# Performance work log

Measured on AMD Instinct MI355X. Metric: run time of the kernel, lower is better.

Reference implementation:

```python
import jax, jax.numpy as jnp
import numpy as np

NUM_SELECT = 300

def _cxcywh_to_xyxy(b):
    cx, cy, w, h = b[..., 0], b[..., 1], b[..., 2], b[..., 3]
    return jnp.stack([cx - w * 0.5, cy - h * 0.5, cx + w * 0.5, cy + h * 0.5], axis=-1)

def setup_inputs() -> dict:
    key = jax.random.key(0)
    k1, k2, k3 = jax.random.split(key, 3)
    B, Q, C = 512, 900, 256
    pred_logits = jax.random.normal(k1, (B, Q, C), dtype=jnp.float32)
    pred_boxes = jax.random.uniform(k2, (B, Q, 4), dtype=jnp.float32)  # normalized cxcywh in [0,1)
    target_sizes = jax.random.uniform(k3, (B, 2), dtype=jnp.float32) * 1333.0 + 1.0  # (h, w)
    return {"pred_logits": pred_logits, "pred_boxes": pred_boxes, "target_sizes": target_sizes}

def reference(pred_logits, pred_boxes, target_sizes):
    B, Q, C = pred_logits.shape
    prob = jax.nn.sigmoid(pred_logits)                      # [B,Q,C]
    flat = prob.reshape(B, Q * C)
    topk_vals, topk_idxs = jax.lax.top_k(flat, NUM_SELECT)  # [B,K]
    scores = topk_vals
    topk_boxes = topk_idxs // C                              # query index
    labels = topk_idxs % C                                   # class index
    out_boxes = _cxcywh_to_xyxy(pred_boxes)                  # [B,Q,4]
    out_boxes = jnp.take_along_axis(out_boxes, topk_boxes[:, :, None], axis=1)  # [B,K,4]
    img_h, img_w = target_sizes[:, 0], target_sizes[:, 1]
    scale = jnp.stack([img_w, img_h, img_w, img_h], axis=1)  # [B,4]
    out_boxes = out_boxes * scale[:, None, :]
    return scores, labels, out_boxes
```

## Files before the change

### kernel.cpp

```cpp
#include <hip/hip_runtime.h>
#include <math.h>


#define NB 512
#define NQ 900
#define NC 256
#define NELEM (NQ*NC)
#define NF4 (NELEM/4)
#define NSEL 300
#define NTHREADS 1024
#define CAP1 6144
#define CAP2 1024
#define SORT_N 1024

__device__ __forceinline__ unsigned keyOf(float f) {
    unsigned u = __float_as_uint(f);
    return u ^ ((unsigned)((int)u >> 31) | 0x80000000u);
}
__device__ __forceinline__ float keyToFloat(unsigned k) {
    unsigned u = (k & 0x80000000u) ? (k ^ 0x80000000u) : ~k;
    return __uint_as_float(u);
}

__global__ __launch_bounds__(NTHREADS) void detpost_kernel(
    const float* __restrict__ logits, const float* __restrict__ boxes,
    const float* __restrict__ tsizes, float* __restrict__ out)
{
    __shared__ uint2 buf1[CAP1];
    __shared__ uint2 buf2[CAP2];
    __shared__ unsigned hist[256];
    __shared__ unsigned sAbove, sCnt, sT, sCand, sDone;

    const int tid  = threadIdx.x;
    const int lane = tid & 63;
    const int row  = blockIdx.x;
    const float4* row4 = (const float4*)(logits + (size_t)row * NELEM);

    unsigned P = 0, pos = 28, T = 0, cand = 0;
    while (true) {
        if (tid < 16) hist[tid] = 0;
        if (tid == 16 % NTHREADS + 16) {}
        if (tid == 17) sAbove = 0;
        __syncthreads();

        unsigned c[16];
        #pragma unroll
        for (int n = 0; n < 16; ++n) c[n] = 0;
        unsigned cAb = 0;
        const unsigned long long upper = (unsigned long long)P + (16ULL << pos);
        unsigned long long acc = 0; int pend = 0;

        for (unsigned i = tid; i < NF4; i += NTHREADS) {
            float4 v = row4[i];
            #pragma unroll
            for (int c4 = 0; c4 < 4; ++c4) {
                float f = (c4 == 0) ? v.x : (c4 == 1) ? v.y : (c4 == 2) ? v.z : v.w;
                unsigned k = keyOf(f);
                if ((unsigned long long)k >= upper) cAb++;
                else if (k >= P) acc += 1ULL << (((k >> pos) & 0xFu) << 2);
            }
            if (++pend == 3) {
                pend = 0;
                #pragma unroll
                for (int n = 0; n < 16; ++n) c[n] += (unsigned)(acc >> (4 * n)) & 0xFu;
                acc = 0;
            }
        }
        #pragma unroll
        for (int n = 0; n < 16; ++n) c[n] += (unsigned)(acc >> (4 * n)) & 0xFu;

        #pragma unroll
        for (int n = 0; n < 16; ++n) {
            unsigned v = c[n];
            for (int off = 32; off; off >>= 1) v += __shfl_down(v, off, 64);
            if (lane == 0 && v) atomicAdd(&hist[n], v);
        }
        {
            unsigned v = cAb;
            for (int off = 32; off; off >>= 1) v += __shfl_down(v, off, 64);
            if (lane == 0 && v) atomicAdd(&sAbove, v);
        }
        __syncthreads();

        if (tid == 0) {
            unsigned run = sAbove; int b = 0;
            for (int n = 15; n >= 0; --n) {
                run += hist[n];
                if (run >= NSEL) { b = n; break; }
            }
            sT = P | ((unsigned)b << pos);
            sCand = run;
            sDone = (run <= CAP1 || pos == 0) ? 1u : 0u;
        }
        __syncthreads();
        T = sT; cand = sCand;
        unsigned done = sDone;
        __syncthreads();
        if (done) break;
        P = T; pos -= 4;
    }

    if (tid == 0) sCnt = 0;
    __syncthreads();
    for (unsigned i = tid; i < NF4; i += NTHREADS) {
        float4 v = row4[i];
        #pragma unroll
        for (int c4 = 0; c4 < 4; ++c4) {
            float f = (c4 == 0) ? v.x : (c4 == 1) ? v.y : (c4 == 2) ? v.z : v.w;
            unsigned k = keyOf(f);
            if (k >= T) {
                unsigned p2 = atomicAdd(&sCnt, 1u);
                if (p2 < CAP1) buf1[p2] = make_uint2(k, i * 4u + (unsigned)c4);
            }
        }
    }
    __syncthreads();
    unsigned cnt = min(sCnt, (unsigned)CAP1);
    (void)cand;

    uint2* src = buf1; uint2* dst = buf2;
    unsigned dstCap = CAP2;
    int p = (int)pos - 8;
    while (cnt > CAP2 && p >= 0) {
        if (tid < 256) hist[tid] = 0;
        if (tid == 0) { sAbove = 0; sCnt = 0; }
        __syncthreads();

        const unsigned Pm = T & (0xFFFFFFFFu << (p + 8));
        const unsigned long long up = (unsigned long long)Pm + (1ULL << (p + 8));
        for (unsigned i = tid; i < cnt; i += NTHREADS) {
            unsigned k = src[i].x;
            if ((unsigned long long)k >= up) atomicAdd(&sAbove, 1u);
            else atomicAdd(&hist[(k >> p) & 0xFFu], 1u);
        }
        __syncthreads();

        if (tid == 0) {
            unsigned run = sAbove; int b = 0;
            for (int n = 255; n >= 0; --n) {
                run += hist[n];
                if (run >= NSEL) { b = n; break; }
            }
            sT = Pm | ((unsigned)b << p);
            sCand = run;
        }
        __syncthreads();
        const unsigned Tn = sT;
        const unsigned newCnt = min(sCand, dstCap);
        for (unsigned i = tid; i < cnt; i += NTHREADS) {
            uint2 e = src[i];
            if (e.x >= Tn) {
                unsigned q = atomicAdd(&sCnt, 1u);
                if (q < dstCap) dst[q] = e;
            }
        }
        __syncthreads();
        T = Tn; cnt = newCnt;
        uint2* t = src; src = dst; dst = t;
        dstCap = (dst == buf1) ? (unsigned)CAP1 : (unsigned)CAP2;
        p -= 8;
    }
    if (cnt > CAP2) cnt = CAP2;

    unsigned long long* zb = (unsigned long long*)buf1;
    {
        unsigned i = tid;
        unsigned long long z = 0;
        if (i < cnt) {
            uint2 e = src[i];
            z = ((unsigned long long)e.x << 32) | (unsigned)(~e.y);
        }
        zb[i] = z;
    }
    __syncthreads();
    for (unsigned kk = 2; kk <= SORT_N; kk <<= 1) {
        for (unsigned j = kk >> 1; j > 0; j >>= 1) {
            unsigned i = tid, ixj = i ^ j;
            if (ixj > i) {
                unsigned long long a = zb[i], bz = zb[ixj];
                bool sw = ((i & kk) == 0) ? (a < bz) : (a > bz);
                if (sw) { zb[i] = bz; zb[ixj] = a; }
            }
            __syncthreads();
        }
    }

    if (tid < NSEL) {
        unsigned long long z = zb[tid];
        unsigned k   = (unsigned)(z >> 32);
        unsigned idx = ~(unsigned)z;
        float f = keyToFloat(k);
        double pd = 1.0 / (1.0 + exp(-(double)f));
        unsigned label = idx & (NC - 1);
        unsigned q = idx >> 8;
        float4 bx = ((const float4*)boxes)[(size_t)row * NQ + q];
        float imh = tsizes[row * 2 + 0];
        float imw = tsizes[row * 2 + 1];
        float x0 = (bx.x - bx.z * 0.5f) * imw;
        float y0 = (bx.y - bx.w * 0.5f) * imh;
        float x1 = (bx.x + bx.z * 0.5f) * imw;
        float y1 = (bx.y + bx.w * 0.5f) * imh;
        out[(size_t)row * NSEL + tid] = (float)pd;
        out[(size_t)NB * NSEL + (size_t)row * NSEL + tid] = (float)label;
        float* ob = out + (size_t)2 * NB * NSEL + ((size_t)row * NSEL + tid) * 4;
        ob[0] = x0; ob[1] = y0; ob[2] = x1; ob[3] = y1;
    }
}

extern "C" void kernel_launch(void* const* d_in, const int* in_sizes, int n_in,
                              void* d_out, int out_size, void* d_ws, size_t ws_size,
                              hipStream_t stream) {
    const float* logits = (const float*)d_in[0];
    const float* boxes  = (const float*)d_in[1];
    const float* tsz    = (const float*)d_in[2];
    float* out = (float*)d_out;
    detpost_kernel<<<NB, NTHREADS, 0, stream>>>(logits, boxes, tsz, out);
}
```

Measured before the change: 715.1 us.

## Replace 4-bit radix select passes with wide 8192-bin LDS histogram select

The multi-pass 4-bit radix select, which reads the full row once per pass, is replaced with a 13-bit (8192-bin) shared-memory histogram built with LDS atomics, followed by a parallel suffix scan to find the threshold bin. For typical logit distributions this should settle the threshold in one pass, so the row is read twice (histogram plus collect) instead of many times. The collect step writes packed 64-bit keys straight into a 2048-entry buffer, removing the shared-memory refinement loop, and the bitonic sort adapts between 1024 and 2048 entries. Loads are manually unrolled four float4s per iteration. The cost is heavy LDS atomic contention on popular bins and a larger sort when there are more than 1024 candidates.

```diff
diff --git a/kernel.cpp b/kernel.cpp
--- a/kernel.cpp
+++ b/kernel.cpp
@@ -8,10 +8,11 @@
 #define NELEM (NQ*NC)
 #define NF4 (NELEM/4)
 #define NSEL 300
-#define NTHREADS 1024
-#define CAP1 6144
-#define CAP2 1024
-#define SORT_N 1024
+#define NT 1024
+#define HBINS 8192
+#define CAP 2048
+
+typedef unsigned long long ull;
 
 __device__ __forceinline__ unsigned keyOf(float f) {
     unsigned u = __float_as_uint(f);
@@ -22,171 +23,132 @@
     return __uint_as_float(u);
 }
 
-__global__ __launch_bounds__(NTHREADS) void detpost_kernel(
+__global__ __launch_bounds__(NT) void detpost_kernel(
     const float* __restrict__ logits, const float* __restrict__ boxes,
     const float* __restrict__ tsizes, float* __restrict__ out)
 {
-    __shared__ uint2 buf1[CAP1];
-    __shared__ uint2 buf2[CAP2];
-    __shared__ unsigned hist[256];
-    __shared__ unsigned sAbove, sCnt, sT, sCand, sDone;
+    __shared__ unsigned hist[HBINS];
+    __shared__ ull zb[CAP];
+    __shared__ unsigned suf[NT];
+    __shared__ unsigned sT, sCand, sAbove, sDone, sCnt;
 
-    const int tid  = threadIdx.x;
-    const int lane = tid & 63;
-    const int row  = blockIdx.x;
-    const float4* row4 = (const float4*)(logits + (size_t)row * NELEM);
+    const int tid = threadIdx.x;
+    const int row = blockIdx.x;
+    const float4* __restrict__ r4 = (const float4*)(logits + (size_t)row * NELEM);
 
-    unsigned P = 0, pos = 28, T = 0, cand = 0;
+    unsigned W0 = 0;
+    unsigned sh = 19;
+    unsigned above = 0;
+    unsigned T, cand;
+
     while (true) {
-        if (tid < 16) hist[tid] = 0;
-        if (tid == 16 % NTHREADS + 16) {}
-        if (tid == 17) sAbove = 0;
+        for (int i = tid; i < HBINS; i += NT) hist[i] = 0;
         __syncthreads();
 
-        unsigned c[16];
-        #pragma unroll
-        for (int n = 0; n < 16; ++n) c[n] = 0;
-        unsigned cAb = 0;
-        const unsigned long long upper = (unsigned long long)P + (16ULL << pos);
-        unsigned long long acc = 0; int pend = 0;
-
-        for (unsigned i = tid; i < NF4; i += NTHREADS) {
-            float4 v = row4[i];
-            #pragma unroll
-            for (int c4 = 0; c4 < 4; ++c4) {
-                float f = (c4 == 0) ? v.x : (c4 == 1) ? v.y : (c4 == 2) ? v.z : v.w;
-                unsigned k = keyOf(f);
-                if ((unsigned long long)k >= upper) cAb++;
-                else if (k >= P) acc += 1ULL << (((k >> pos) & 0xFu) << 2);
-            }
-            if (++pend == 3) {
-                pend = 0;
-                #pragma unroll
-                for (int n = 0; n < 16; ++n) c[n] += (unsigned)(acc >> (4 * n)) & 0xFu;
-                acc = 0;
-            }
+        unsigned i0 = tid;
+        #pragma unroll 1
+        for (int it = 0; it < 14; ++it, i0 += 4096) {
+            float4 a = r4[i0];
+            float4 b = r4[i0 + 1024];
+            float4 c = r4[i0 + 2048];
+            float4 d = r4[i0 + 3072];
+            #define PH(f) { unsigned k = keyOf(f); unsigned bin = (k - W0) >> sh; \
+                            if (bin < HBINS) atomicAdd(&hist[bin], 1u); }
+            PH(a.x) PH(a.y) PH(a.z) PH(a.w)
+            PH(b.x) PH(b.y) PH(b.z) PH(b.w)
+            PH(c.x) PH(c.y) PH(c.z) PH(c.w)
+            PH(d.x) PH(d.y) PH(d.z) PH(d.w)
         }
-        #pragma unroll
-        for (int n = 0; n < 16; ++n) c[n] += (unsigned)(acc >> (4 * n)) & 0xFu;
-
-        #pragma unroll
-        for (int n = 0; n < 16; ++n) {
-            unsigned v = c[n];
-            for (int off = 32; off; off >>= 1) v += __shfl_down(v, off, 64);
-            if (lane == 0 && v) atomicAdd(&hist[n], v);
-        }
-        {
-            unsigned v = cAb;
-            for (int off = 32; off; off >>= 1) v += __shfl_down(v, off, 64);
-            if (lane == 0 && v) atomicAdd(&sAbove, v);
+        if (tid < 256) {
+            float4 a = r4[57344 + tid];
+            PH(a.x) PH(a.y) PH(a.z) PH(a.w)
         }
         __syncthreads();
 
-        if (tid == 0) {
-            unsigned run = sAbove; int b = 0;
-            for (int n = 15; n >= 0; --n) {
-                run += hist[n];
-                if (run >= NSEL) { b = n; break; }
+        unsigned local = 0;
+        #pragma unroll
+        for (int j = 0; j < 8; ++j) local += hist[tid * 8 + j];
+        suf[tid] = local;
+        __syncthreads();
+        for (int off = 1; off < NT; off <<= 1) {
+            unsigned v = suf[tid] + ((tid + off < NT) ? suf[tid + off] : 0u);
+            __syncthreads();
+            suf[tid] = v;
+            __syncthreads();
+        }
+        unsigned mySuf = suf[tid];
+        unsigned nxt = (tid < NT - 1) ? suf[tid + 1] : 0u;
+        if (above + mySuf >= NSEL && above + nxt < NSEL) {
+            unsigned run = above + nxt;
+            for (int j = 7; j >= 0; --j) {
+                unsigned h = hist[tid * 8 + j];
+                run += h;
+                if (run >= NSEL) {
+                    sT = W0 + ((unsigned)(tid * 8 + j) << sh);
+                    sCand = run;
+                    sAbove = run - h;
+                    sDone = (run <= CAP || sh == 0) ? 1u : 0u;
+                    break;
+                }
             }
-            sT = P | ((unsigned)b << pos);
-            sCand = run;
-            sDone = (run <= CAP1 || pos == 0) ? 1u : 0u;
         }
         __syncthreads();
         T = sT; cand = sCand;
-        unsigned done = sDone;
+        if (sDone) break;
+        above = sAbove;
+        W0 = T;
+        sh = (sh >= 13) ? (sh - 13) : 0u;
         __syncthreads();
-        if (done) break;
-        P = T; pos -= 4;
     }
+    (void)cand;
 
     if (tid == 0) sCnt = 0;
     __syncthreads();
-    for (unsigned i = tid; i < NF4; i += NTHREADS) {
-        float4 v = row4[i];
-        #pragma unroll
-        for (int c4 = 0; c4 < 4; ++c4) {
-            float f = (c4 == 0) ? v.x : (c4 == 1) ? v.y : (c4 == 2) ? v.z : v.w;
-            unsigned k = keyOf(f);
-            if (k >= T) {
-                unsigned p2 = atomicAdd(&sCnt, 1u);
-                if (p2 < CAP1) buf1[p2] = make_uint2(k, i * 4u + (unsigned)c4);
-            }
+    {
+        unsigned i0 = tid;
+        #pragma unroll 1
+        for (int it = 0; it < 14; ++it, i0 += 4096) {
+            float4 a = r4[i0];
+            float4 b = r4[i0 + 1024];
+            float4 c = r4[i0 + 2048];
+            float4 d = r4[i0 + 3072];
+            #define PC(f, ei) { unsigned k = keyOf(f); if (k >= T) { \
+                unsigned p = atomicAdd(&sCnt, 1u); \
+                if (p < CAP) zb[p] = ((ull)k << 32) | (unsigned)~(unsigned)(ei); } }
+            PC(a.x, i0*4+0)          PC(a.y, i0*4+1)          PC(a.z, i0*4+2)          PC(a.w, i0*4+3)
+            PC(b.x, (i0+1024)*4+0)   PC(b.y, (i0+1024)*4+1)   PC(b.z, (i0+1024)*4+2)   PC(b.w, (i0+1024)*4+3)
+            PC(c.x, (i0+2048)*4+0)   PC(c.y, (i0+2048)*4+1)   PC(c.z, (i0+2048)*4+2)   PC(c.w, (i0+2048)*4+3)
+            PC(d.x, (i0+3072)*4+0)   PC(d.y, (i0+3072)*4+1)   PC(d.z, (i0+3072)*4+2)   PC(d.w, (i0+3072)*4+3)
+        }
+        if (tid < 256) {
+            float4 a = r4[57344 + tid];
+            unsigned e0 = (57344 + tid) * 4;
+            PC(a.x, e0+0) PC(a.y, e0+1) PC(a.z, e0+2) PC(a.w, e0+3)
         }
     }
     __syncthreads();
-    unsigned cnt = min(sCnt, (unsigned)CAP1);
-    (void)cand;
+    unsigned cnt = min(sCnt, (unsigned)CAP);
 
-    uint2* src = buf1; uint2* dst = buf2;
-    unsigned dstCap = CAP2;
-    int p = (int)pos - 8;
-    while (cnt > CAP2 && p >= 0) {
-        if (tid < 256) hist[tid] = 0;
-        if (tid == 0) { sAbove = 0; sCnt = 0; }
-        __syncthreads();
-
-        const unsigned Pm = T & (0xFFFFFFFFu << (p + 8));
-        const unsigned long long up = (unsigned long long)Pm + (1ULL << (p + 8));
-        for (unsigned i = tid; i < cnt; i += NTHREADS) {
-            unsigned k = src[i].x;
-            if ((unsigned long long)k >= up) atomicAdd(&sAbove, 1u);
-            else atomicAdd(&hist[(k >> p) & 0xFFu], 1u);
-        }
-        __syncthreads();
-
-        if (tid == 0) {
-            unsigned run = sAbove; int b = 0;
-            for (int n = 255; n >= 0; --n) {
-                run += hist[n];
-                if (run >= NSEL) { b = n; break; }
-            }
-            sT = Pm | ((unsigned)b << p);
-            sCand = run;
-        }
-        __syncthreads();
-        const unsigned Tn = sT;
-        const unsigned newCnt = min(sCand, dstCap);
-        for (unsigned i = tid; i < cnt; i += NTHREADS) {
-            uint2 e = src[i];
-            if (e.x >= Tn) {
-                unsigned q = atomicAdd(&sCnt, 1u);
-                if (q < dstCap) dst[q] = e;
-            }
-        }
-        __syncthreads();
-        T = Tn; cnt = newCnt;
-        uint2* t = src; src = dst; dst = t;
-        dstCap = (dst == buf1) ? (unsigned)CAP1 : (unsigned)CAP2;
-        p -= 8;
-    }
-    if (cnt > CAP2) cnt = CAP2;
-
-    unsigned long long* zb = (unsigned long long*)buf1;
-    {
-        unsigned i = tid;
-        unsigned long long z = 0;
-        if (i < cnt) {
-            uint2 e = src[i];
-            z = ((unsigned long long)e.x << 32) | (unsigned)(~e.y);
-        }
-        zb[i] = z;
-    }
+    unsigned nSort = (cnt <= 1024u) ? 1024u : (unsigned)CAP;
+    for (unsigned i = tid; i < nSort; i += NT)
+        if (i >= cnt) zb[i] = 0ULL;
     __syncthreads();
-    for (unsigned kk = 2; kk <= SORT_N; kk <<= 1) {
+    for (unsigned kk = 2; kk <= nSort; kk <<= 1) {
         for (unsigned j = kk >> 1; j > 0; j >>= 1) {
-            unsigned i = tid, ixj = i ^ j;
-            if (ixj > i) {
-                unsigned long long a = zb[i], bz = zb[ixj];
-                bool sw = ((i & kk) == 0) ? (a < bz) : (a > bz);
-                if (sw) { zb[i] = bz; zb[ixj] = a; }
+            for (unsigned i = tid; i < nSort; i += NT) {
+                unsigned ixj = i ^ j;
+                if (ixj > i) {
+                    ull A = zb[i], B = zb[ixj];
+                    bool sw = ((i & kk) == 0) ? (A < B) : (A > B);
+                    if (sw) { zb[i] = B; zb[ixj] = A; }
+                }
             }
             __syncthreads();
         }
     }
 
     if (tid < NSEL) {
-        unsigned long long z = zb[tid];
+        ull z = zb[tid];
         unsigned k   = (unsigned)(z >> 32);
         unsigned idx = ~(unsigned)z;
         float f = keyToFloat(k);
@@ -214,5 +176,5 @@
     const float* boxes  = (const float*)d_in[1];
     const float* tsz    = (const float*)d_in[2];
     float* out = (float*)d_out;
-    detpost_kernel<<<NB, NTHREADS, 0, stream>>>(logits, boxes, tsz, out);
+    detpost_kernel<<<NB, NT, 0, stream>>>(logits, boxes, tsz, out);
 }
```

Result: faster. 690.4 us (-3.5%).
